# Optimization experiments

Measured on AMD Instinct MI355X. Metric: run time of the kernel, lower is better.

The kernel has to match this reference:

```python
import jax, jax.numpy as jnp
import numpy as np
from jax import lax

N, M, K, D = 2048, 64, 32, 512
C = 1.0


def setup_inputs() -> dict:
    key = jax.random.key(0)
    k1, k2, k3, k4 = jax.random.split(key, 4)
    W = jax.random.normal(k1, (K, D), dtype=jnp.float32) * 0.05
    T = jax.random.normal(k2, (K, K), dtype=jnp.float32) * 0.05
    data = jax.random.normal(k3, (N, M, D), dtype=jnp.float32)
    labels = jax.random.randint(k4, (N, M), 0, K, dtype=jnp.int32)
    return {"W": W, "T": T, "data": data, "labels": labels}


def _crf_word(W, T, data, labels):
    # data: [m, d], labels: [m] int. dots: [m, K] emission scores.
    dots = data @ W.T
    m = dots.shape[0]
    k = T.shape[0]

    # alpha[i, k] = logsumexp_j(dots[i-1, j] + alpha[i-1, j] + T[j, k]); alpha[0] = 0
    def alpha_step(prev, d_prev):
        a = jax.nn.logsumexp(prev[:, None] + d_prev[:, None] + T, axis=0)
        return a, a
    _, alphas = lax.scan(alpha_step, jnp.zeros((k,), dots.dtype), dots[:-1])
    alpha = jnp.concatenate([jnp.zeros((1, k), dots.dtype), alphas], axis=0)  # [m, K]

    # beta[i, k] = logsumexp_j(dots[i+1, j] + beta[i+1, j] + T[k, j]); beta[m-1] = 0
    def beta_step(prev, d_next):
        b = jax.nn.logsumexp(prev[None, :] + d_next[None, :] + T, axis=1)
        return b, b
    _, betas = lax.scan(beta_step, jnp.zeros((k,), dots.dtype), dots[1:][::-1])
    beta = jnp.concatenate([betas[::-1], jnp.zeros((1, k), dots.dtype)], axis=0)  # [m, K]

    # unary marginals p1 [m, K]
    p1 = jax.nn.softmax(alpha + beta + dots, axis=-1)
    # pairwise marginals p2 [m-1, K, K]; softmax over flattened KxK per position
    s = (alpha[:-1] + dots[:-1])[:, :, None] + (beta[1:] + dots[1:])[:, None, :] + T[None, :, :]
    p2 = jax.nn.softmax(s.reshape(m - 1, k * k), axis=-1).reshape(m - 1, k, k)

    # log P(y|x)
    logZ = jax.nn.logsumexp(dots[-1] + alpha[-1])
    emit = jnp.take_along_axis(dots, labels[:, None], axis=1).sum()
    trans = T[labels[:-1], labels[1:]].sum()
    logpyx = emit + trans - logZ

    # analytic gradients (as computed by the module, not autodiff)
    onehot = jax.nn.one_hot(labels, k, dtype=dots.dtype)          # [m, K]
    dw = (onehot - p1).T @ data                                    # [K, d]
    trans_oh = onehot[:-1][:, :, None] * onehot[1:][:, None, :]    # [m-1, K, K]
    dT = (trans_oh - p2).sum(axis=0)                               # [K, K]
    return logpyx, dw, dT


def reference(W, T, data, labels):
    logpyx, dw, dT = jax.vmap(_crf_word, in_axes=(None, None, 0, 0))(W, T, data, labels)
    meandw = dw.mean(axis=0)
    meandT = dT.mean(axis=0)
    gradients = jnp.concatenate([meandw.ravel(), meandT.ravel()])
    # objValue (stored on the module) -- computed for faithfulness though forward returns gradients
    obj = -C * logpyx.mean() + 0.5 * jnp.sum(W ** 2) + 0.5 * jnp.sum(T ** 2)
    del obj
    return gradients
```

## Files before the change

### kernel.cpp

```cpp
#include <hip/hip_runtime.h>
#include <math.h>

typedef __bf16 bf16x8 __attribute__((ext_vector_type(8)));
typedef float f32x4 __attribute__((ext_vector_type(4)));

__device__ __forceinline__ bf16x8 to_bf16x8(float4 a, float4 b) {
    bf16x8 r;
    r[0] = (__bf16)a.x; r[1] = (__bf16)a.y; r[2] = (__bf16)a.z; r[3] = (__bf16)a.w;
    r[4] = (__bf16)b.x; r[5] = (__bf16)b.y; r[6] = (__bf16)b.z; r[7] = (__bf16)b.w;
    return r;
}
#define MFMA16(A, B, C) __builtin_amdgcn_mfma_f32_16x16x32_bf16((A), (B), (C), 0, 0, 0)

__device__ __forceinline__ float rl(float v, int j) {
    return __int_as_float(__builtin_amdgcn_readlane(__float_as_int(v), j));
}

__device__ __forceinline__ float dpp_sum32(float v) {
    float f = v;
    f += __int_as_float(__builtin_amdgcn_update_dpp(0, __float_as_int(f), 0x111, 0xf, 0xf, true));
    f += __int_as_float(__builtin_amdgcn_update_dpp(0, __float_as_int(f), 0x112, 0xf, 0xf, true));
    f += __int_as_float(__builtin_amdgcn_update_dpp(0, __float_as_int(f), 0x114, 0xf, 0xf, true));
    f += __int_as_float(__builtin_amdgcn_update_dpp(0, __float_as_int(f), 0x118, 0xf, 0xf, true));
    f += __int_as_float(__builtin_amdgcn_update_dpp(0, __float_as_int(f), 0x142, 0xa, 0xf, false));
    return rl(f, 31);
}

#define RL_MATVEC(T, EV, OUT)                                                  \
    {                                                                          \
        float a0_ = 0.f, a1_ = 0.f, a2_ = 0.f, a3_ = 0.f;                      \
        _Pragma("unroll") for (int j_ = 0; j_ < 32; j_ += 4) {                 \
            a0_ += EV[j_ + 0] * rl((T), j_ + 0);                               \
            a1_ += EV[j_ + 1] * rl((T), j_ + 1);                               \
            a2_ += EV[j_ + 2] * rl((T), j_ + 2);                               \
            a3_ += EV[j_ + 3] * rl((T), j_ + 3);                               \
        }                                                                      \
        OUT = (a0_ + a1_) + (a2_ + a3_);                                       \
    }

__global__ __launch_bounds__(256) void k_prep(const float* __restrict__ W,
                                              bf16x8* __restrict__ wsW) {
    const int e = blockIdx.x * 256 + threadIdx.x;
    const int gk = e >> 7, h = (e >> 6) & 1, l = e & 63;
    const float* src = W + (size_t)(h * 16 + (l & 15)) * 512 + gk * 32 + (l >> 4) * 8;
    float4 lo = *(const float4*)src, hi = *(const float4*)(src + 4);
    wsW[e] = to_bf16x8(lo, hi);
}

__global__ __launch_bounds__(128) void k_word(const float* __restrict__ data,
                                              const bf16x8* __restrict__ wsW,
                                              const float* __restrict__ Tm,
                                              const int* __restrict__ labels,
                                              float* __restrict__ Pdiff,
                                              float* __restrict__ dTpart) {
    __shared__ __align__(16) __bf16 gdb[2048];
    __shared__ __align__(16) __bf16 Unb[2048];
    __shared__ __align__(16) __bf16 Mb[2048];
    __shared__ float Sb[1024];
    __shared__ float bscale[64];
    __shared__ int lab[64];

    const int n = blockIdx.x;
    const int tid = threadIdx.x;
    const int wv = tid >> 6;
    const int lane = tid & 63;
    const int k = tid & 31;
    float* drow = Pdiff + (size_t)n * 2048;

    {
        const int m16 = lane & 15;
        const int kb = lane >> 4;
        const size_t row0 = (size_t)n * 64 + wv * 32;
        const float* arow0 = data + (row0 + m16) * 512 + kb * 8;
        const float* arow1 = arow0 + 16 * 512;

        f32x4 acc00 = {0.f, 0.f, 0.f, 0.f}, acc01 = {0.f, 0.f, 0.f, 0.f};
        f32x4 acc10 = {0.f, 0.f, 0.f, 0.f}, acc11 = {0.f, 0.f, 0.f, 0.f};

#pragma unroll 2
        for (int kk = 0; kk < 16; ++kk) {
            const int off = kk * 32;
            float4 a0l = *(const float4*)(arow0 + off);
            float4 a0h = *(const float4*)(arow0 + off + 4);
            float4 a1l = *(const float4*)(arow1 + off);
            float4 a1h = *(const float4*)(arow1 + off + 4);
            bf16x8 a0 = to_bf16x8(a0l, a0h), a1 = to_bf16x8(a1l, a1h);
            bf16x8 b0 = wsW[kk * 128 + lane];
            bf16x8 b1 = wsW[kk * 128 + 64 + lane];
            acc00 = MFMA16(a0, b0, acc00);
            acc01 = MFMA16(a0, b1, acc01);
            acc10 = MFMA16(a1, b0, acc10);
            acc11 = MFMA16(a1, b1, acc11);
        }
        const int ib = wv * 32 + kb * 4;
#pragma unroll
        for (int r = 0; r < 4; ++r) {
            gdb[(ib + r) * 32 + m16]           = (__bf16)__expf(acc00[r]);
            gdb[(ib + r) * 32 + 16 + m16]      = (__bf16)__expf(acc01[r]);
            gdb[(ib + 16 + r) * 32 + m16]      = (__bf16)__expf(acc10[r]);
            gdb[(ib + 16 + r) * 32 + 16 + m16] = (__bf16)__expf(acc11[r]);
        }
    }
#pragma unroll
    for (int i = 0; i < 8; ++i) Sb[tid * 8 + i] = 0.f;
    if (tid < 64) { lab[tid] = labels[n * 64 + tid]; bscale[tid] = 1.f; }
    __syncthreads();

    if (wv == 0) {
        float Ecol[32];
#pragma unroll
        for (int j = 0; j < 32; ++j) Ecol[j] = __expf(Tm[j * 32 + k]);
        float Areg = 1.f;
        float gdc = (float)gdb[k];
#pragma unroll 1
        for (int g = 0; g < 16; ++g) {
#pragma unroll
            for (int ii = 0; ii < 4; ++ii) {
                const int i = g * 4 + ii;
                float t = Areg * gdc;
                Unb[i * 32 + k] = (__bf16)t;
                if (i < 63) {
                    gdc = (float)gdb[(i + 1) * 32 + k];
                    float anew;
                    RL_MATVEC(t, Ecol, anew);
                    Areg = anew;
                }
            }
            if (g < 15) Areg *= __builtin_amdgcn_rcpf(rl(Areg, 0));
        }
    } else {
        float Erow[32];
#pragma unroll
        for (int j = 0; j < 32; ++j) Erow[j] = __expf(Tm[k * 32 + j]);
        float Mreg = 1.f;
        Mb[63 * 32 + k] = (__bf16)1.f;
        float gdc = (float)gdb[63 * 32 + k];
#pragma unroll 1
        for (int g = 0; g < 16; ++g) {
#pragma unroll
            for (int ii = 0; ii < 4; ++ii) {
                const int s = g * 4 + ii;
                if (s < 63) {
                    const int i = 63 - s;
                    float ww = gdc * Mreg;
                    gdc = (float)gdb[(i - 1) * 32 + k];
                    float m2;
                    RL_MATVEC(ww, Erow, m2);
                    Mb[(i - 1) * 32 + k] = (__bf16)m2;
                    Mreg = m2;
                }
            }
            if (g < 15) {
                float rc = __builtin_amdgcn_rcpf(rl(Mreg, 0));
                Mreg *= rc;
                if (lane == 0) bscale[58 - 4 * g] = rc;
            }
        }
    }
    __syncthreads();

    float Scol[32];
#pragma unroll
    for (int j = 0; j < 32; ++j) Scol[j] = 0.f;
    const int i0 = wv * 32;
    float un = (float)Unb[i0 * 32 + k];
    float mm = (float)Mb[i0 * 32 + k];
#pragma unroll 1
    for (int s = 0; s < 32; ++s) {
        const int i = i0 + s;
        float gd_n = 0.f, mb_n = 0.f, un_n = 0.f;
        if (i < 63) {
            gd_n = (float)gdb[(i + 1) * 32 + k];
            mb_n = (float)Mb[(i + 1) * 32 + k];
            un_n = (float)Unb[(i + 1) * 32 + k];
        }
        float t = un * mm;
        float Z = dpp_sum32(t);
        float rZ = __builtin_amdgcn_rcpf(Z);
        float pd = ((lab[i] == k) ? 1.f : 0.f) - t * rZ;
        if (lane < 32) drow[i * 32 + k] = pd;
        if (i < 63) {
            float f = gd_n * mb_n * rZ * bscale[i];
#pragma unroll
            for (int j = 0; j < 32; j += 4) {
                Scol[j + 0] += rl(un, j + 0) * f;
                Scol[j + 1] += rl(un, j + 1) * f;
                Scol[j + 2] += rl(un, j + 2) * f;
                Scol[j + 3] += rl(un, j + 3) * f;
            }
        }
        un = un_n; mm = mb_n;
    }
    if (lane < 32) {
#pragma unroll
        for (int j = 0; j < 32; ++j) atomicAdd(&Sb[j * 32 + k], Scol[j]);
    }
    __syncthreads();

    float* op = dTpart + (size_t)n * 1024;
#pragma unroll
    for (int e = 0; e < 8; ++e) {
        const int idx = tid * 8 + e;
        op[idx] = -__expf(Tm[idx]) * Sb[idx];
    }
    __syncthreads();
    if (tid < 63) atomicAdd(&op[lab[tid] * 32 + lab[tid + 1]], 1.0f);
}

__global__ __launch_bounds__(256) void k_dw(const float* __restrict__ data,
                                            const float* __restrict__ Pd,
                                            float* __restrict__ dwp) {
    const int g = blockIdx.x >> 2;
    const int q = blockIdx.x & 3;
    const int tid = threadIdx.x;
    const int kg = __builtin_amdgcn_readfirstlane(tid >> 6);
    const int lane = tid & 63;
    const int k0 = kg << 3;
    const int d0 = q * 128 + lane * 2;

    float2 acc[8];
#pragma unroll
    for (int i = 0; i < 8; ++i) acc[i] = make_float2(0.f, 0.f);

    const size_t rbase = (size_t)g * 512;
    const float* dptr = data + rbase * 512 + d0;
    const float4* pptr = (const float4*)(Pd + rbase * 32) + kg * 2;

#define FMA8_2(PA, PB, DV)                                                     \
    acc[0].x += (PA).x * (DV).x; acc[0].y += (PA).x * (DV).y;                  \
    acc[1].x += (PA).y * (DV).x; acc[1].y += (PA).y * (DV).y;                  \
    acc[2].x += (PA).z * (DV).x; acc[2].y += (PA).z * (DV).y;                  \
    acc[3].x += (PA).w * (DV).x; acc[3].y += (PA).w * (DV).y;                  \
    acc[4].x += (PB).x * (DV).x; acc[4].y += (PB).x * (DV).y;                  \
    acc[5].x += (PB).y * (DV).x; acc[5].y += (PB).y * (DV).y;                  \
    acc[6].x += (PB).z * (DV).x; acc[6].y += (PB).z * (DV).y;                  \
    acc[7].x += (PB).w * (DV).x; acc[7].y += (PB).w * (DV).y;

    for (int r = 0; r < 512; r += 4) {
        float2 dv0 = *(const float2*)(dptr + (size_t)(r + 0) * 512);
        float2 dv1 = *(const float2*)(dptr + (size_t)(r + 1) * 512);
        float2 dv2 = *(const float2*)(dptr + (size_t)(r + 2) * 512);
        float2 dv3 = *(const float2*)(dptr + (size_t)(r + 3) * 512);
        float4 pa0 = pptr[(r + 0) * 8], pb0 = pptr[(r + 0) * 8 + 1];
        float4 pa1 = pptr[(r + 1) * 8], pb1 = pptr[(r + 1) * 8 + 1];
        float4 pa2 = pptr[(r + 2) * 8], pb2 = pptr[(r + 2) * 8 + 1];
        float4 pa3 = pptr[(r + 3) * 8], pb3 = pptr[(r + 3) * 8 + 1];
        FMA8_2(pa0, pb0, dv0)
        FMA8_2(pa1, pb1, dv1)
        FMA8_2(pa2, pb2, dv2)
        FMA8_2(pa3, pb3, dv3)
    }
#undef FMA8_2

    float* op = dwp + (size_t)g * 16384;
#pragma unroll
    for (int kk = 0; kk < 8; ++kk)
        *(float2*)(op + (k0 + kk) * 512 + d0) = acc[kk];
}

__global__ __launch_bounds__(256) void k_final(const float* __restrict__ dwp,
                                               const float* __restrict__ dTp,
                                               float* __restrict__ out) {
    __shared__ float red[256];
    const int b = blockIdx.x, t = threadIdx.x;
    const float inv = 1.0f / 2048.0f;
    if (b < 256) {
        const int q = t >> 6, ol = t & 63;
        const int oi = b * 64 + ol;
        float s = 0.f;
#pragma unroll 4
        for (int j = 0; j < 64; ++j) s += dwp[(size_t)(q * 64 + j) * 16384 + oi];
        red[t] = s;
        __syncthreads();
        if (t < 64) out[b * 64 + t] = (red[t] + red[t + 64] + red[t + 128] + red[t + 192]) * inv;
    } else {
        const int ol = t >> 4, q = t & 15;
        const int oi = (b - 256) * 16 + ol;
        float s = 0.f;
#pragma unroll 4
        for (int j = 0; j < 128; ++j) s += dTp[(size_t)(q * 128 + j) * 1024 + oi];
        s += __shfl_xor(s, 1, 16); s += __shfl_xor(s, 2, 16);
        s += __shfl_xor(s, 4, 16); s += __shfl_xor(s, 8, 16);
        if (q == 0) out[16384 + oi] = s * inv;
    }
}

extern "C" void kernel_launch(void* const* d_in, const int* in_sizes, int n_in,
                              void* d_out, int out_size, void* d_ws, size_t ws_size,
                              hipStream_t stream) {
    const float* W = (const float*)d_in[0];
    const float* Tm = (const float*)d_in[1];
    const float* data = (const float*)d_in[2];
    const int* labels = (const int*)d_in[3];
    float* out = (float*)d_out;
    float* ws = (float*)d_ws;

    float* Pdiff = ws;
    float* dTpart = ws + 4194304;
    float* dwpart = ws + 6291456;
    bf16x8* wsW = (bf16x8*)(ws + 10485760);

    hipLaunchKernelGGL(k_prep, dim3(8), dim3(256), 0, stream, W, wsW);
    hipLaunchKernelGGL(k_word, dim3(2048), dim3(128), 0, stream,
                       data, wsW, Tm, labels, Pdiff, dTpart);
    hipLaunchKernelGGL(k_dw, dim3(1024), dim3(256), 0, stream, data, Pdiff, dwpart);
    hipLaunchKernelGGL(k_final, dim3(320), dim3(256), 0, stream, dwpart, dTpart, out);
}
```

Measured before the change: 213.2 us.

## Fuse marginal and dT accumulation into second half of forward/backward recursions

Splits the alpha and beta recursions at the midpoint with a barrier. After it, each wave computes unary marginals, drow entries and the rank-1 dT accumulation for its half of positions inline with the remaining recursion steps. This replaces the separate post-recursion pass that re-read Unb/Mb from shared memory, and overlaps marginal work with the serial chain. The cost is more work inside the latency-bound recursion loop and more register pressure from holding Scol alongside Ecol/Erow.

```diff
diff --git a/kernel.cpp b/kernel.cpp
--- a/kernel.cpp
+++ b/kernel.cpp
@@ -36,6 +36,16 @@
             a3_ += EV[j_ + 3] * rl((T), j_ + 3);                               \
         }                                                                      \
         OUT = (a0_ + a1_) + (a2_ + a3_);                                       \
+    }
+
+#define RANK1(U, F, SC)                                                        \
+    {                                                                          \
+        _Pragma("unroll") for (int j_ = 0; j_ < 32; j_ += 4) {                 \
+            SC[j_ + 0] += rl((U), j_ + 0) * (F);                               \
+            SC[j_ + 1] += rl((U), j_ + 1) * (F);                               \
+            SC[j_ + 2] += rl((U), j_ + 2) * (F);                               \
+            SC[j_ + 3] += rl((U), j_ + 3) * (F);                               \
+        }                                                                      \
     }
 
 __global__ __launch_bounds__(256) void k_prep(const float* __restrict__ W,
@@ -106,6 +116,10 @@
     if (tid < 64) { lab[tid] = labels[n * 64 + tid]; bscale[tid] = 1.f; }
     __syncthreads();
 
+    float Scol[32];
+#pragma unroll
+    for (int j = 0; j < 32; ++j) Scol[j] = 0.f;
+
     if (wv == 0) {
         float Ecol[32];
 #pragma unroll
@@ -113,17 +127,44 @@
         float Areg = 1.f;
         float gdc = (float)gdb[k];
 #pragma unroll 1
-        for (int g = 0; g < 16; ++g) {
+        for (int g = 0; g < 8; ++g) {
 #pragma unroll
             for (int ii = 0; ii < 4; ++ii) {
                 const int i = g * 4 + ii;
                 float t = Areg * gdc;
                 Unb[i * 32 + k] = (__bf16)t;
+                gdc = (float)gdb[(i + 1) * 32 + k];
+                float anew;
+                RL_MATVEC(t, Ecol, anew);
+                Areg = anew;
+            }
+            Areg *= __builtin_amdgcn_rcpf(rl(Areg, 0));
+        }
+        __syncthreads();
+#pragma unroll 1
+        for (int g = 8; g < 16; ++g) {
+#pragma unroll
+            for (int ii = 0; ii < 4; ++ii) {
+                const int i = g * 4 + ii;
+                float t = Areg * gdc;
+                Unb[i * 32 + k] = (__bf16)t;
+                float mm = (float)Mb[i * 32 + k];
+                float gdn = 0.f, mbn = 0.f;
                 if (i < 63) {
-                    gdc = (float)gdb[(i + 1) * 32 + k];
+                    gdn = (float)gdb[(i + 1) * 32 + k];
+                    mbn = (float)Mb[(i + 1) * 32 + k];
+                }
+                float Z = dpp_sum32(t * mm);
+                float rZ = __builtin_amdgcn_rcpf(Z);
+                float pd = ((lab[i] == k) ? 1.f : 0.f) - t * mm * rZ;
+                if (lane < 32) drow[i * 32 + k] = pd;
+                if (i < 63) {
+                    float f = gdn * mbn * rZ * bscale[i];
+                    RANK1(t, f, Scol);
                     float anew;
                     RL_MATVEC(t, Ecol, anew);
                     Areg = anew;
+                    gdc = gdn;
                 }
             }
             if (g < 15) Areg *= __builtin_amdgcn_rcpf(rl(Areg, 0));
@@ -135,19 +176,62 @@
         float Mreg = 1.f;
         Mb[63 * 32 + k] = (__bf16)1.f;
         float gdc = (float)gdb[63 * 32 + k];
+        float mst = 1.f;
 #pragma unroll 1
-        for (int g = 0; g < 16; ++g) {
+        for (int g = 0; g < 8; ++g) {
+#pragma unroll
+            for (int ii = 0; ii < 4; ++ii) {
+                const int s = g * 4 + ii;
+                const int i = 63 - s;
+                float ww = gdc * Mreg;
+                gdc = (float)gdb[(i - 1) * 32 + k];
+                float m2;
+                RL_MATVEC(ww, Erow, m2);
+                Mb[(i - 1) * 32 + k] = (__bf16)m2;
+                Mreg = m2;
+                mst = m2;
+            }
+            {
+                float rc = __builtin_amdgcn_rcpf(rl(Mreg, 0));
+                Mreg *= rc;
+                if (lane == 0) bscale[58 - 4 * g] = rc;
+            }
+        }
+        __syncthreads();
+        {
+            float un = (float)Unb[31 * 32 + k];
+            float mbn = (float)Mb[32 * 32 + k];
+            float gdn = (float)gdb[32 * 32 + k];
+            float Z = dpp_sum32(un * mst);
+            float rZ = __builtin_amdgcn_rcpf(Z);
+            float pd = ((lab[31] == k) ? 1.f : 0.f) - un * mst * rZ;
+            if (lane < 32) drow[31 * 32 + k] = pd;
+            float f = gdn * mbn * rZ;
+            RANK1(un, f, Scol);
+        }
+#pragma unroll 1
+        for (int g = 8; g < 16; ++g) {
 #pragma unroll
             for (int ii = 0; ii < 4; ++ii) {
                 const int s = g * 4 + ii;
                 if (s < 63) {
                     const int i = 63 - s;
-                    float ww = gdc * Mreg;
-                    gdc = (float)gdb[(i - 1) * 32 + k];
+                    const int p = i - 1;
+                    float gd_i = gdc;
+                    float ww = gd_i * Mreg;
+                    gdc = (float)gdb[p * 32 + k];
                     float m2;
                     RL_MATVEC(ww, Erow, m2);
-                    Mb[(i - 1) * 32 + k] = (__bf16)m2;
+                    Mb[p * 32 + k] = (__bf16)m2;
+                    float un = (float)Unb[p * 32 + k];
+                    float Z = dpp_sum32(un * m2);
+                    float rZ = __builtin_amdgcn_rcpf(Z);
+                    float pd = ((lab[p] == k) ? 1.f : 0.f) - un * m2 * rZ;
+                    if (lane < 32) drow[p * 32 + k] = pd;
+                    float f = gd_i * mst * rZ * bscale[p];
+                    RANK1(un, f, Scol);
                     Mreg = m2;
+                    mst = m2;
                 }
             }
             if (g < 15) {
@@ -156,40 +240,6 @@
                 if (lane == 0) bscale[58 - 4 * g] = rc;
             }
         }
-    }
-    __syncthreads();
-
-    float Scol[32];
-#pragma unroll
-    for (int j = 0; j < 32; ++j) Scol[j] = 0.f;
-    const int i0 = wv * 32;
-    float un = (float)Unb[i0 * 32 + k];
-    float mm = (float)Mb[i0 * 32 + k];
-#pragma unroll 1
-    for (int s = 0; s < 32; ++s) {
-        const int i = i0 + s;
-        float gd_n = 0.f, mb_n = 0.f, un_n = 0.f;
-        if (i < 63) {
-            gd_n = (float)gdb[(i + 1) * 32 + k];
-            mb_n = (float)Mb[(i + 1) * 32 + k];
-            un_n = (float)Unb[(i + 1) * 32 + k];
-        }
-        float t = un * mm;
-        float Z = dpp_sum32(t);
-        float rZ = __builtin_amdgcn_rcpf(Z);
-        float pd = ((lab[i] == k) ? 1.f : 0.f) - t * rZ;
-        if (lane < 32) drow[i * 32 + k] = pd;
-        if (i < 63) {
-            float f = gd_n * mb_n * rZ * bscale[i];
-#pragma unroll
-            for (int j = 0; j < 32; j += 4) {
-                Scol[j + 0] += rl(un, j + 0) * f;
-                Scol[j + 1] += rl(un, j + 1) * f;
-                Scol[j + 2] += rl(un, j + 2) * f;
-                Scol[j + 3] += rl(un, j + 3) * f;
-            }
-        }
-        un = un_n; mm = mb_n;
     }
     if (lane < 32) {
 #pragma unroll
```

Result: faster. 207.6 us, median of 2 (-2.6%).
